# Kernel tuning notes

Measured on AMD Instinct MI355X. Metric: run time of the kernel, lower is better.

The kernel has to match this reference:

```python
import jax, jax.numpy as jnp
import numpy as np

HEADS, LEVELS, POINTS, DIMS = 8, 4, 4, 256
CH = DIMS // HEADS
SHAPES = np.array([[96, 96], [48, 48], [24, 24], [12, 12]], dtype=np.int64)
LEVEL_START = np.concatenate([[0], np.cumsum(SHAPES[:, 0] * SHAPES[:, 1])[:-1]]).astype(np.int64)
HW = int((SHAPES[:, 0] * SHAPES[:, 1]).sum())
N, Q = 2, HW


def setup_inputs() -> dict:
    key = jax.random.key(0)
    ks = jax.random.split(key, 8)
    return {
        "q": jax.random.normal(ks[0], (N, Q, DIMS), jnp.float32),
        "p": jax.random.uniform(ks[1], (N, Q, LEVELS, 2), jnp.float32),
        "v": jax.random.normal(ks[2], (N, HW, DIMS), jnp.float32),
        "W_off": jax.random.normal(ks[3], (DIMS, HEADS * LEVELS * POINTS * 2), jnp.float32) * 0.01,
        "b_off": jax.random.normal(ks[4], (HEADS * LEVELS * POINTS * 2,), jnp.float32) * 0.5,
        "W_attn": jax.random.normal(ks[5], (DIMS, HEADS * LEVELS * POINTS), jnp.float32) * 0.02,
        "b_attn": jnp.zeros((HEADS * LEVELS * POINTS,), jnp.float32),
        "W_in": jax.random.normal(ks[6], (DIMS, DIMS), jnp.float32) / np.float32(np.sqrt(DIMS)),
        "b_in": jnp.zeros((DIMS,), jnp.float32),
        "W_out": jax.random.normal(ks[7], (DIMS, DIMS), jnp.float32) / np.float32(np.sqrt(DIMS)),
        "b_out": jnp.zeros((DIMS,), jnp.float32),
        "shapes": jnp.asarray(SHAPES),
        "level_index": jnp.asarray(LEVEL_START),
    }


def _sample_level(vl, loc_l, Hl, Wl):
    """Bilinear sample with zero padding outside the feature map.
    vl: [N, Hl*Wl, heads, C]; loc_l: [N, Q, heads, P, 2] normalized (x, y) in [0,1].
    Returns [N, Q, P, heads, C]."""
    Nb, Qn, Hd, P, _ = loc_l.shape
    x = loc_l[..., 0] * Wl - 0.5  # pixel coords, align_corners=False convention
    y = loc_l[..., 1] * Hl - 0.5
    x0 = jnp.floor(x)
    y0 = jnp.floor(y)
    dx = x - x0
    dy = y - y0
    x0i = x0.astype(jnp.int32)
    y0i = y0.astype(jnp.int32)
    out = jnp.zeros((Nb, Qn, P, Hd, vl.shape[-1]), vl.dtype)
    corners = ((x0i, y0i, (1 - dx) * (1 - dy)), (x0i + 1, y0i, dx * (1 - dy)),
               (x0i, y0i + 1, (1 - dx) * dy), (x0i + 1, y0i + 1, dx * dy))
    for cx, cy, w in corners:
        valid = (cx >= 0) & (cx < Wl) & (cy >= 0) & (cy < Hl)
        idx = jnp.clip(cy, 0, Hl - 1) * Wl + jnp.clip(cx, 0, Wl - 1)  # [N,Q,Hd,P]
        idx_t = idx.transpose(0, 1, 3, 2).reshape(Nb, Qn * P, Hd, 1)
        g = jnp.take_along_axis(vl, idx_t, axis=1).reshape(Nb, Qn, P, Hd, -1)
        wv = jnp.where(valid, w, 0.0).transpose(0, 1, 3, 2)  # [N,Q,P,Hd]
        out = out + g * wv[..., None].astype(vl.dtype)
    return out


def _forward(q, p, v, W_off, b_off, W_attn, b_attn, W_in, b_in, W_out, b_out, shp, lsi):
    Nb, Qn, _ = q.shape
    v = (v @ W_in + b_in).reshape(Nb, -1, HEADS, CH)
    off = (q @ W_off + b_off).reshape(Nb, Qn, HEADS, LEVELS, POINTS, 2)
    attn = jax.nn.softmax((q @ W_attn + b_attn).reshape(Nb, Qn, HEADS, LEVELS * POINTS), axis=-1)
    attn = attn.reshape(Nb, Qn, HEADS, LEVELS, POINTS)
    # offsets normalized by (W, H) of each level, added to reference points (2-coord branch)
    off_norm = jnp.asarray(np.stack([shp[:, 1], shp[:, 0]], -1), q.dtype)  # [L, 2]
    loc = p[:, :, None, :, None, :] + off / off_norm[None, None, None, :, None, :]  # [N,Q,Hd,L,P,2]
    out = jnp.zeros((Nb, Qn, HEADS, CH), q.dtype)
    for l in range(LEVELS):
        Hl, Wl = int(shp[l, 0]), int(shp[l, 1])
        s = int(lsi[l])
        vl = jax.lax.slice_in_dim(v, s, s + Hl * Wl, axis=1)
        samp = _sample_level(vl, loc[:, :, :, l], Hl, Wl)  # [N,Q,P,Hd,C]
        out = out + jnp.einsum('nqphc,nqhp->nqhc', samp, attn[:, :, :, l])
    return out.reshape(Nb, Qn, DIMS) @ W_out + b_out


def reference(q, p, v, W_off, b_off, W_attn, b_attn, W_in, b_in, W_out, b_out, shapes, level_index):
    shp = np.asarray(shapes)  # spatial shapes are structural constants
    lsi = np.asarray(level_index)
    return _forward(q, p, v, W_off, b_off, W_attn, b_attn, W_in, b_in, W_out, b_out, shp, lsi)
```

## Files before the change

### kernel.cpp

```cpp
#include <hip/hip_runtime.h>
#include <hip/hip_bf16.h>
#include <math.h>

#define NB      2
#define QN      12240
#define HW_TOT  12240
#define DIMS    256
#define HEADS   8
#define CH      32
#define LEVELS  4
#define POINTS  4
#define M_TOT   (NB * QN)

typedef unsigned short ushort_t;
typedef __attribute__((ext_vector_type(8))) short short8;
typedef __attribute__((ext_vector_type(4))) float floatx4;

__device__ __forceinline__ ushort_t f2bf(float f) {
    __hip_bfloat16 h = __float2bfloat16(f);
    return *reinterpret_cast<ushort_t*>(&h);
}

__global__ __launch_bounds__(256) void convert_qv_kernel(
    const float* __restrict__ v, const float* __restrict__ q,
    ushort_t* __restrict__ vbf, ushort_t* __restrict__ qbf)
{
    const size_t i = ((size_t)blockIdx.x * 256 + threadIdx.x) * 8;
    const size_t half = (size_t)M_TOT * DIMS;
    const float* src; ushort_t* dst; size_t off;
    if (i < half) { src = v; dst = vbf; off = i; }
    else          { src = q; dst = qbf; off = i - half; }
    const float4 a = *(const float4*)&src[off];
    const float4 b = *(const float4*)&src[off + 4];
    ushort_t t[8] = {f2bf(a.x), f2bf(a.y), f2bf(a.z), f2bf(a.w),
                     f2bf(b.x), f2bf(b.y), f2bf(b.z), f2bf(b.w)};
    *(int4*)&dst[off] = *(int4*)t;
}

__global__ __launch_bounds__(256) void prep_weights_kernel(
    const float* __restrict__ W_in, const float* __restrict__ W_off,
    const float* __restrict__ W_attn, const float* __restrict__ W_out,
    const float* __restrict__ b_off, const float* __restrict__ b_attn,
    ushort_t* __restrict__ Tin, ushort_t* __restrict__ Tcomb,
    ushort_t* __restrict__ Tout, float* __restrict__ bcomb,
    int* __restrict__ vpad)
{
    const int z  = blockIdx.z;
    const int gi = blockIdx.x * 256 + threadIdx.x;
    if (z == 0 && gi < 32) vpad[gi] = 0;
    if (z == 1 && gi < 384)
        bcomb[gi] = (gi < 256) ? b_off[gi] : b_attn[gi - 256];
    const int Nw = (z == 1) ? 384 : 256;
    if (gi >= Nw * 256) return;
    const int k = gi & 255;
    const int n = gi >> 8;
    float val; ushort_t* T;
    if (z == 0)      { val = W_in[k * 256 + n];  T = Tin;  }
    else if (z == 1) { val = (n < 256) ? W_off[k * 256 + n]
                                       : W_attn[k * 128 + (n - 256)]; T = Tcomb; }
    else             { val = W_out[k * 256 + n]; T = Tout; }
    T[n * 256 + k] = f2bf(val);
}

__device__ __forceinline__ void gemm_tile_core(
    const ushort_t* __restrict__ A, const ushort_t* __restrict__ BT,
    const float* __restrict__ bias, void* __restrict__ C, bool c_bf16,
    int M, int Nc, int bm0, int bn0, int K,
    ushort_t* As, ushort_t* Bs)
{
    const int tid  = threadIdx.x;
    const int wave = tid >> 6;
    const int lane = tid & 63;
    const int quad = lane >> 4;
    const int l16  = lane & 15;
    const int wm   = (wave >> 1) * 64;
    const int wn   = (wave & 1) * 64;

    const int off0 = tid * 16;
    const int row0 = off0 >> 6;
    const int kc0  = (off0 & 63) >> 1;

    int ar0 = bm0 + row0;      if (ar0 > M - 1) ar0 = M - 1;
    int ar1 = bm0 + row0 + 64; if (ar1 > M - 1) ar1 = M - 1;

    const ushort_t* ga0 = A  + (size_t)ar0 * K + kc0;
    const ushort_t* ga1 = A  + (size_t)ar1 * K + kc0;
    const ushort_t* gb0 = BT + (size_t)(bn0 + row0) * K + kc0;
    const ushort_t* gb1 = BT + (size_t)(bn0 + row0 + 64) * K + kc0;

    ushort_t* lA0 = As + wave * 512;
    ushort_t* lA1 = As + wave * 512 + 2048;
    ushort_t* lB0 = Bs + wave * 512;
    ushort_t* lB1 = Bs + wave * 512 + 2048;

    floatx4 acc[4][4];
    #pragma unroll
    for (int i = 0; i < 4; ++i)
        #pragma unroll
        for (int j = 0; j < 4; ++j)
            acc[i][j] = (floatx4){0.f, 0.f, 0.f, 0.f};

    for (int kk = 0; kk < K; kk += 32) {
        __builtin_amdgcn_global_load_lds(
            (const __attribute__((address_space(1))) void*)(ga0 + kk),
            (__attribute__((address_space(3))) void*)lA0, 16, 0, 0);
        __builtin_amdgcn_global_load_lds(
            (const __attribute__((address_space(1))) void*)(ga1 + kk),
            (__attribute__((address_space(3))) void*)lA1, 16, 0, 0);
        __builtin_amdgcn_global_load_lds(
            (const __attribute__((address_space(1))) void*)(gb0 + kk),
            (__attribute__((address_space(3))) void*)lB0, 16, 0, 0);
        __builtin_amdgcn_global_load_lds(
            (const __attribute__((address_space(1))) void*)(gb1 + kk),
            (__attribute__((address_space(3))) void*)lB1, 16, 0, 0);
        __syncthreads();

        short8 af[4], bfr[4];
        #pragma unroll
        for (int mt = 0; mt < 4; ++mt)
            af[mt] = *(const short8*)&As[(wm + mt * 16 + l16) * 32 + quad * 8];
        #pragma unroll
        for (int nt = 0; nt < 4; ++nt)
            bfr[nt] = *(const short8*)&Bs[(wn + nt * 16 + l16) * 32 + quad * 8];
        #pragma unroll
        for (int mt = 0; mt < 4; ++mt)
            #pragma unroll
            for (int nt = 0; nt < 4; ++nt)
                acc[mt][nt] = __builtin_amdgcn_mfma_f32_16x16x32_bf16(
                    af[mt], bfr[nt], acc[mt][nt], 0, 0, 0);
        __syncthreads();
    }

    #pragma unroll
    for (int mt = 0; mt < 4; ++mt) {
        #pragma unroll
        for (int j = 0; j < 4; ++j) {
            const int row = bm0 + wm + mt * 16 + quad * 4 + j;
            if (row >= M) continue;
            #pragma unroll
            for (int nt = 0; nt < 4; ++nt) {
                const int col = bn0 + wn + nt * 16 + l16;
                const float val = acc[mt][nt][j] + bias[col];
                if (c_bf16) {
                    const size_t idx = (((size_t)(col >> 5) * M + row) << 5) + (col & 31);
                    ((ushort_t*)C)[idx] = f2bf(val);
                } else {
                    ((float*)C)[(size_t)row * Nc + col] = val;
                }
            }
        }
    }
}

__global__ __launch_bounds__(256) void gemm_proj_kernel(
    const ushort_t* __restrict__ vbf, const ushort_t* __restrict__ qbf,
    const ushort_t* __restrict__ Tin, const ushort_t* __restrict__ Tcomb,
    const float* __restrict__ b_in, const float* __restrict__ bcomb,
    ushort_t* __restrict__ vproj, float* __restrict__ offlog)
{
    __shared__ ushort_t As[128 * 32];
    __shared__ ushort_t Bs[128 * 32];
    const int bm0 = blockIdx.x * 128;
    const int y = blockIdx.y;
    if (y < 2)
        gemm_tile_core(vbf, Tin, b_in, vproj, true, M_TOT, 256, bm0, y * 128, 256, As, Bs);
    else
        gemm_tile_core(qbf, Tcomb, bcomb, offlog, false, M_TOT, 384, bm0, (y - 2) * 128, 256, As, Bs);
}

__global__ __launch_bounds__(256) void gemm_out_kernel(
    const ushort_t* __restrict__ mid, const ushort_t* __restrict__ Tout,
    const float* __restrict__ b_out, float* __restrict__ out)
{
    __shared__ ushort_t As[128 * 32];
    __shared__ ushort_t Bs[128 * 32];
    gemm_tile_core(mid, Tout, b_out, out, false, M_TOT, 256,
                   blockIdx.x * 128, blockIdx.y * 128, 256, As, Bs);
}

#define LO32(u) __uint_as_float((u) << 16)
#define HI32(u) __uint_as_float((u) & 0xffff0000u)
#define ACC8(W, g) \
    a0 = fmaf(W, LO32(g.x), a0);  a1 = fmaf(W, HI32(g.x), a1); \
    a2 = fmaf(W, LO32(g.y), a2);  a3 = fmaf(W, HI32(g.y), a3); \
    a4 = fmaf(W, LO32(g.z), a4);  a5 = fmaf(W, HI32(g.z), a5); \
    a6 = fmaf(W, LO32(g.w), a6);  a7 = fmaf(W, HI32(g.w), a7);

__global__ __launch_bounds__(256, 8) void msda_sample_kernel(
    const ushort_t* __restrict__ vproj, const float* __restrict__ offlog,
    const float* __restrict__ p, ushort_t* __restrict__ mid)
{
    __shared__ int s_buf[4096];

    const int tid = threadIdx.x;
    const int wv  = tid >> 6;
    const int l   = tid & 63;
    const int nq  = blockIdx.x * 4 + wv;
    const int nb  = (nq >= QN) ? 1 : 0;
    const int wbase = wv * 1024;

    const size_t orow = (size_t)nq * 384;
    const float2 off0 = *(const float2*)&offlog[orow + 2 * l];
    const float2 off1 = *(const float2*)&offlog[orow + 128 + 2 * l];
    const float  lg0  = offlog[orow + 256 + l];
    const float  lg1  = offlog[orow + 320 + l];
    const int    lvl  = (l >> 2) & 3;
    const float2 pl   = *(const float2*)&p[(size_t)nq * 8 + lvl * 2];

    float m0 = lg0, m1 = lg1;
    #pragma unroll
    for (int m = 8; m; m >>= 1) {
        m0 = fmaxf(m0, __shfl_xor(m0, m));
        m1 = fmaxf(m1, __shfl_xor(m1, m));
    }
    const float e0 = __expf(lg0 - m0);
    const float e1 = __expf(lg1 - m1);
    float s0 = e0, s1 = e1;
    #pragma unroll
    for (int m = 8; m; m >>= 1) {
        s0 += __shfl_xor(s0, m);
        s1 += __shfl_xor(s1, m);
    }
    const float wt0 = e0 * __builtin_amdgcn_rcpf(s0);
    const float wt1 = e1 * __builtin_amdgcn_rcpf(s1);

    const int   Wl  = 96 >> lvl;
    const float fW  = (float)Wl;
    const int   st  = 12288 - (12288 >> (2 * lvl));
    const int   h4  = l >> 4;

    #pragma unroll
    for (int set = 0; set < 2; ++set) {
        const float ox = set ? off1.x : off0.x;
        const float oy = set ? off1.y : off0.y;
        const float wt = set ? wt1 : wt0;
        const int   h  = set ? (h4 + 4) : h4;

        const float x  = fmaf(pl.x, fW, ox) - 0.5f;
        const float y  = fmaf(pl.y, fW, oy) - 0.5f;
        const float xf = floorf(x), yf = floorf(y);
        const float dx = x - xf,    dy = y - yf;
        const int   x0 = (int)xf,   y0 = (int)yf;
        const bool vxl = (unsigned)x0       < (unsigned)Wl;
        const bool vxr = (unsigned)(x0 + 1) < (unsigned)Wl;
        const bool vy0 = (unsigned)y0       < (unsigned)Wl;
        const bool vy1 = (unsigned)(y0 + 1) < (unsigned)Wl;

        const float wxl = vxl ? (1.0f - dx) : (vxr ? dx : 0.0f);
        const float wxr = (vxl && vxr) ? dx : 0.0f;
        const int   xb  = vxl ? x0 : 0;

        const float wy0f = wt * (1.0f - dy), wy1f = wt * dy;
        const float w_l0 = vy0 ? wxl * wy0f : 0.0f;
        const float w_r0 = vy0 ? wxr * wy0f : 0.0f;
        const float w_l1 = vy1 ? wxl * wy1f : 0.0f;
        const float w_r1 = vy1 ? wxr * wy1f : 0.0f;

        int yc0 = y0;     if (yc0 < 0) yc0 = 0; if (yc0 > Wl - 1) yc0 = Wl - 1;
        int yc1 = y0 + 1; if (yc1 < 0) yc1 = 0; if (yc1 > Wl - 1) yc1 = Wl - 1;

        const int rowb = h * M_TOT + nb * HW_TOT + st + xb;
        const int lin0 = rowb + yc0 * Wl;
        const int lin1 = rowb + yc1 * Wl;

        const int a  = l * 16 + set * 8;
        const int ph = (a ^ (((a >> 8) & 3) << 2)) + wbase;
        *(int4*)&s_buf[ph] = (int4){lin0 << 6, __float_as_int(w_l0),
                                    __float_as_int(w_r0), lin1 << 6};
        *(int2*)&s_buf[ph ^ 4] = (int2){__float_as_int(w_l1), __float_as_int(w_r1)};
    }

    __builtin_amdgcn_wave_barrier();
    asm volatile("s_waitcnt lgkmcnt(0)" ::: "memory");
    __builtin_amdgcn_wave_barrier();

    const int  h    = l >> 3;
    const int  c16  = (l & 7) * 16;
    const bool hicn = (l & 4) != 0;
    const int  rbas = (h & 3) * 256 + (h >> 2) * 8;
    const char* __restrict__ vb = (const char*)vproj;

    float a0 = 0.f, a1 = 0.f, a2 = 0.f, a3 = 0.f;
    float a4 = 0.f, a5 = 0.f, a6 = 0.f, a7 = 0.f;

    #pragma unroll 2
    for (int t = 0; t < 16; ++t) {
        const int ia = rbas + t * 16;
        const int ph = (ia ^ (((ia >> 8) & 3) << 2)) + wbase;
        const int4 cA = *(const int4*)&s_buf[ph];
        const int2 cB = *(const int2*)&s_buf[ph ^ 4];
        const uint4 g0 = *(const uint4*)(vb + (unsigned)(cA.x + c16));
        const uint4 g1 = *(const uint4*)(vb + (unsigned)(cA.w + c16));
        const float w0 = hicn ? __int_as_float(cA.z) : __int_as_float(cA.y);
        const float w1 = hicn ? __int_as_float(cB.y) : __int_as_float(cB.x);
        ACC8(w0, g0);
        ACC8(w1, g1);
    }

    a0 += __shfl_xor(a0, 4);  a1 += __shfl_xor(a1, 4);
    a2 += __shfl_xor(a2, 4);  a3 += __shfl_xor(a3, 4);
    a4 += __shfl_xor(a4, 4);  a5 += __shfl_xor(a5, 4);
    a6 += __shfl_xor(a6, 4);  a7 += __shfl_xor(a7, 4);

    const float o0 = hicn ? a4 : a0;
    const float o1 = hicn ? a5 : a1;
    const float o2 = hicn ? a6 : a2;
    const float o3 = hicn ? a7 : a3;
    ushort_t mv[4] = {f2bf(o0), f2bf(o1), f2bf(o2), f2bf(o3)};
    const int col = h * 32 + (l & 3) * 8 + (l & 4);
    *(uint2*)&mid[(size_t)nq * 256 + col] = *(uint2*)mv;
}

extern "C" void kernel_launch(void* const* d_in, const int* in_sizes, int n_in,
                              void* d_out, int out_size, void* d_ws, size_t ws_size,
                              hipStream_t stream)
{
    const float* q      = (const float*)d_in[0];
    const float* p      = (const float*)d_in[1];
    const float* v      = (const float*)d_in[2];
    const float* W_off  = (const float*)d_in[3];
    const float* b_off  = (const float*)d_in[4];
    const float* W_attn = (const float*)d_in[5];
    const float* b_attn = (const float*)d_in[6];
    const float* W_in   = (const float*)d_in[7];
    const float* b_in   = (const float*)d_in[8];
    const float* W_out  = (const float*)d_in[9];
    const float* b_out  = (const float*)d_in[10];
    float* out = (float*)d_out;

    const int M = M_TOT;

    ushort_t* vproj  = (ushort_t*)d_ws;
    ushort_t* vpad   = vproj + (size_t)M * 256;
    float*    offlog = (float*)(vpad + 64);
    ushort_t* vbf    = (ushort_t*)(offlog + (size_t)M * 384);
    ushort_t* mid    = vbf;
    ushort_t* qbf    = vbf + (size_t)M * 256;
    ushort_t* Tin    = qbf + (size_t)M * 256;
    ushort_t* Tcomb  = Tin + 256 * 256;
    ushort_t* Tout   = Tcomb + 384 * 256;
    float*    bcomb  = (float*)(Tout + 256 * 256);

    convert_qv_kernel<<<dim3(6120), 256, 0, stream>>>(v, q, vbf, qbf);
    prep_weights_kernel<<<dim3(384, 1, 3), 256, 0, stream>>>(
        W_in, W_off, W_attn, W_out, b_off, b_attn, Tin, Tcomb, Tout, bcomb,
        (int*)vpad);

    gemm_proj_kernel<<<dim3(192, 5), 256, 0, stream>>>(
        vbf, qbf, Tin, Tcomb, b_in, bcomb, vproj, offlog);
    msda_sample_kernel<<<dim3(M / 4), 256, 0, stream>>>(vproj, offlog, p, mid);
    gemm_out_kernel<<<dim3(192, 2), 256, 0, stream>>>(mid, Tout, b_out, out);
}
```

Measured before the change: 188.7 us.

## Fuse prep kernels, store offsets in fp16, split sampling by head halves

Merges the activation conversion and weight-prep launches into one kernel. The offset/logit projection is now written as fp16 instead of fp32, halving that intermediate's traffic. The sampling kernel is restructured so each block handles half the heads for four queries, doubling the grid, with a padded shared layout and one gather per lane per iteration instead of two. Storing offsets in fp16 loses precision in the sampling coordinates, and the extra shuffle reduction adds work.

```diff
diff --git a/kernel.cpp b/kernel.cpp
--- a/kernel.cpp
+++ b/kernel.cpp
@@ -1,5 +1,6 @@
 #include <hip/hip_runtime.h>
 #include <hip/hip_bf16.h>
+#include <hip/hip_fp16.h>
 #include <math.h>
 
 #define NB      2
@@ -20,24 +21,14 @@
     __hip_bfloat16 h = __float2bfloat16(f);
     return *reinterpret_cast<ushort_t*>(&h);
 }
-
-__global__ __launch_bounds__(256) void convert_qv_kernel(
+__device__ __forceinline__ ushort_t f2h(float f) {
+    __half h = __float2half(f);
+    return *reinterpret_cast<ushort_t*>(&h);
+}
+
+__global__ __launch_bounds__(256) void convert_prep_kernel(
     const float* __restrict__ v, const float* __restrict__ q,
-    ushort_t* __restrict__ vbf, ushort_t* __restrict__ qbf)
-{
-    const size_t i = ((size_t)blockIdx.x * 256 + threadIdx.x) * 8;
-    const size_t half = (size_t)M_TOT * DIMS;
-    const float* src; ushort_t* dst; size_t off;
-    if (i < half) { src = v; dst = vbf; off = i; }
-    else          { src = q; dst = qbf; off = i - half; }
-    const float4 a = *(const float4*)&src[off];
-    const float4 b = *(const float4*)&src[off + 4];
-    ushort_t t[8] = {f2bf(a.x), f2bf(a.y), f2bf(a.z), f2bf(a.w),
-                     f2bf(b.x), f2bf(b.y), f2bf(b.z), f2bf(b.w)};
-    *(int4*)&dst[off] = *(int4*)t;
-}
-
-__global__ __launch_bounds__(256) void prep_weights_kernel(
+    ushort_t* __restrict__ vbf, ushort_t* __restrict__ qbf,
     const float* __restrict__ W_in, const float* __restrict__ W_off,
     const float* __restrict__ W_attn, const float* __restrict__ W_out,
     const float* __restrict__ b_off, const float* __restrict__ b_attn,
@@ -45,26 +36,41 @@
     ushort_t* __restrict__ Tout, float* __restrict__ bcomb,
     int* __restrict__ vpad)
 {
-    const int z  = blockIdx.z;
-    const int gi = blockIdx.x * 256 + threadIdx.x;
-    if (z == 0 && gi < 32) vpad[gi] = 0;
-    if (z == 1 && gi < 384)
-        bcomb[gi] = (gi < 256) ? b_off[gi] : b_attn[gi - 256];
-    const int Nw = (z == 1) ? 384 : 256;
-    if (gi >= Nw * 256) return;
+    const int bx  = blockIdx.x;
+    const int tid = threadIdx.x;
+    if (bx < 6120) {
+        const size_t i = ((size_t)bx * 256 + tid) * 8;
+        const size_t half = (size_t)M_TOT * DIMS;
+        const float* src; ushort_t* dst; size_t off;
+        if (i < half) { src = v; dst = vbf; off = i; }
+        else          { src = q; dst = qbf; off = i - half; }
+        const float4 a = *(const float4*)&src[off];
+        const float4 b = *(const float4*)&src[off + 4];
+        ushort_t t[8] = {f2bf(a.x), f2bf(a.y), f2bf(a.z), f2bf(a.w),
+                         f2bf(b.x), f2bf(b.y), f2bf(b.z), f2bf(b.w)};
+        *(int4*)&dst[off] = *(int4*)t;
+        return;
+    }
+    const int bi = bx - 6120;
+    const int gi = bi * 256 + tid;
+    if (gi < 32)  vpad[gi] = 0;
+    if (gi < 384) bcomb[gi] = (gi < 256) ? b_off[gi] : b_attn[gi - 256];
     const int k = gi & 255;
     const int n = gi >> 8;
-    float val; ushort_t* T;
-    if (z == 0)      { val = W_in[k * 256 + n];  T = Tin;  }
-    else if (z == 1) { val = (n < 256) ? W_off[k * 256 + n]
-                                       : W_attn[k * 128 + (n - 256)]; T = Tcomb; }
-    else             { val = W_out[k * 256 + n]; T = Tout; }
-    T[n * 256 + k] = f2bf(val);
+    if (gi < 65536) {
+        Tin[n * 256 + k]  = f2bf(W_in[k * 256 + n]);
+        Tout[n * 256 + k] = f2bf(W_out[k * 256 + n]);
+    }
+    {
+        const float val = (n < 256) ? W_off[k * 256 + n]
+                                    : W_attn[k * 128 + (n - 256)];
+        Tcomb[n * 256 + k] = f2bf(val);
+    }
 }
 
 __device__ __forceinline__ void gemm_tile_core(
     const ushort_t* __restrict__ A, const ushort_t* __restrict__ BT,
-    const float* __restrict__ bias, void* __restrict__ C, bool c_bf16,
+    const float* __restrict__ bias, void* __restrict__ C, int cmode,
     int M, int Nc, int bm0, int bn0, int K,
     ushort_t* As, ushort_t* Bs)
 {
@@ -141,9 +147,11 @@
             for (int nt = 0; nt < 4; ++nt) {
                 const int col = bn0 + wn + nt * 16 + l16;
                 const float val = acc[mt][nt][j] + bias[col];
-                if (c_bf16) {
+                if (cmode == 1) {
                     const size_t idx = (((size_t)(col >> 5) * M + row) << 5) + (col & 31);
                     ((ushort_t*)C)[idx] = f2bf(val);
+                } else if (cmode == 2) {
+                    ((ushort_t*)C)[(size_t)row * Nc + col] = f2h(val);
                 } else {
                     ((float*)C)[(size_t)row * Nc + col] = val;
                 }
@@ -156,16 +164,16 @@
     const ushort_t* __restrict__ vbf, const ushort_t* __restrict__ qbf,
     const ushort_t* __restrict__ Tin, const ushort_t* __restrict__ Tcomb,
     const float* __restrict__ b_in, const float* __restrict__ bcomb,
-    ushort_t* __restrict__ vproj, float* __restrict__ offlog)
+    ushort_t* __restrict__ vproj, ushort_t* __restrict__ offh)
 {
     __shared__ ushort_t As[128 * 32];
     __shared__ ushort_t Bs[128 * 32];
     const int bm0 = blockIdx.x * 128;
     const int y = blockIdx.y;
     if (y < 2)
-        gemm_tile_core(vbf, Tin, b_in, vproj, true, M_TOT, 256, bm0, y * 128, 256, As, Bs);
+        gemm_tile_core(vbf, Tin, b_in, vproj, 1, M_TOT, 256, bm0, y * 128, 256, As, Bs);
     else
-        gemm_tile_core(qbf, Tcomb, bcomb, offlog, false, M_TOT, 384, bm0, (y - 2) * 128, 256, As, Bs);
+        gemm_tile_core(qbf, Tcomb, bcomb, offh, 2, M_TOT, 384, bm0, (y - 2) * 128, 256, As, Bs);
 }
 
 __global__ __launch_bounds__(256) void gemm_out_kernel(
@@ -174,7 +182,7 @@
 {
     __shared__ ushort_t As[128 * 32];
     __shared__ ushort_t Bs[128 * 32];
-    gemm_tile_core(mid, Tout, b_out, out, false, M_TOT, 256,
+    gemm_tile_core(mid, Tout, b_out, out, 0, M_TOT, 256,
                    blockIdx.x * 128, blockIdx.y * 128, 256, As, Bs);
 }
 
@@ -187,57 +195,48 @@
     a6 = fmaf(W, LO32(g.w), a6);  a7 = fmaf(W, HI32(g.w), a7);
 
 __global__ __launch_bounds__(256, 8) void msda_sample_kernel(
-    const ushort_t* __restrict__ vproj, const float* __restrict__ offlog,
+    const ushort_t* __restrict__ vproj, const ushort_t* __restrict__ offh,
     const float* __restrict__ p, ushort_t* __restrict__ mid)
 {
-    __shared__ int s_buf[4096];
+    __shared__ int4 s_main[4][68];
+    __shared__ int2 s_aux[4][68];
 
     const int tid = threadIdx.x;
     const int wv  = tid >> 6;
     const int l   = tid & 63;
-    const int nq  = blockIdx.x * 4 + wv;
+    const int idx = blockIdx.x;
+    const int b8  = idx & 7;
+    const int hh  = b8 >> 2;
+    const int qg  = (idx >> 3) * 4 + (b8 & 3);
+    const int nq  = qg * 4 + wv;
     const int nb  = (nq >= QN) ? 1 : 0;
-    const int wbase = wv * 1024;
 
     const size_t orow = (size_t)nq * 384;
-    const float2 off0 = *(const float2*)&offlog[orow + 2 * l];
-    const float2 off1 = *(const float2*)&offlog[orow + 128 + 2 * l];
-    const float  lg0  = offlog[orow + 256 + l];
-    const float  lg1  = offlog[orow + 320 + l];
-    const int    lvl  = (l >> 2) & 3;
-    const float2 pl   = *(const float2*)&p[(size_t)nq * 8 + lvl * 2];
-
-    float m0 = lg0, m1 = lg1;
+    const __half2 o2 = *(const __half2*)&offh[orow + hh * 128 + 2 * l];
+    const float2  of = __half22float2(o2);
+    const float   lg = __half2float(
+        *(const __half*)&offh[orow + 256 + hh * 64 + l]);
+    const int     lvl = (l >> 2) & 3;
+    const float2  pl  = *(const float2*)&p[(size_t)nq * 8 + lvl * 2];
+
+    float mx = lg;
     #pragma unroll
-    for (int m = 8; m; m >>= 1) {
-        m0 = fmaxf(m0, __shfl_xor(m0, m));
-        m1 = fmaxf(m1, __shfl_xor(m1, m));
-    }
-    const float e0 = __expf(lg0 - m0);
-    const float e1 = __expf(lg1 - m1);
-    float s0 = e0, s1 = e1;
+    for (int m = 8; m; m >>= 1) mx = fmaxf(mx, __shfl_xor(mx, m));
+    const float e = __expf(lg - mx);
+    float ss = e;
     #pragma unroll
-    for (int m = 8; m; m >>= 1) {
-        s0 += __shfl_xor(s0, m);
-        s1 += __shfl_xor(s1, m);
-    }
-    const float wt0 = e0 * __builtin_amdgcn_rcpf(s0);
-    const float wt1 = e1 * __builtin_amdgcn_rcpf(s1);
-
-    const int   Wl  = 96 >> lvl;
-    const float fW  = (float)Wl;
-    const int   st  = 12288 - (12288 >> (2 * lvl));
-    const int   h4  = l >> 4;
-
-    #pragma unroll
-    for (int set = 0; set < 2; ++set) {
-        const float ox = set ? off1.x : off0.x;
-        const float oy = set ? off1.y : off0.y;
-        const float wt = set ? wt1 : wt0;
-        const int   h  = set ? (h4 + 4) : h4;
-
-        const float x  = fmaf(pl.x, fW, ox) - 0.5f;
-        const float y  = fmaf(pl.y, fW, oy) - 0.5f;
+    for (int m = 8; m; m >>= 1) ss += __shfl_xor(ss, m);
+    const float wt = e * __builtin_amdgcn_rcpf(ss);
+
+    const int   Wl = 96 >> lvl;
+    const float fW = (float)Wl;
+    const int   st = 12288 - (12288 >> (2 * lvl));
+    const int   h4 = l >> 4;
+    const int   h  = hh * 4 + h4;
+
+    {
+        const float x  = fmaf(pl.x, fW, of.x) - 0.5f;
+        const float y  = fmaf(pl.y, fW, of.y) - 0.5f;
         const float xf = floorf(x), yf = floorf(y);
         const float dx = x - xf,    dy = y - yf;
         const int   x0 = (int)xf,   y0 = (int)yf;
@@ -262,53 +261,53 @@
         const int rowb = h * M_TOT + nb * HW_TOT + st + xb;
         const int lin0 = rowb + yc0 * Wl;
         const int lin1 = rowb + yc1 * Wl;
-
-        const int a  = l * 16 + set * 8;
-        const int ph = (a ^ (((a >> 8) & 3) << 2)) + wbase;
-        *(int4*)&s_buf[ph] = (int4){lin0 << 6, __float_as_int(w_l0),
-                                    __float_as_int(w_r0), lin1 << 6};
-        *(int2*)&s_buf[ph ^ 4] = (int2){__float_as_int(w_l1), __float_as_int(w_r1)};
+        const int e17 = h4 * 17 + (l & 15);
+        s_main[wv][e17] = (int4){lin0 << 6, __float_as_int(w_l0),
+                                 __float_as_int(w_r0), lin1 << 6};
+        s_aux[wv][e17]  = (int2){__float_as_int(w_l1), __float_as_int(w_r1)};
     }
 
     __builtin_amdgcn_wave_barrier();
     asm volatile("s_waitcnt lgkmcnt(0)" ::: "memory");
     __builtin_amdgcn_wave_barrier();
 
-    const int  h    = l >> 3;
-    const int  c16  = (l & 7) * 16;
-    const bool hicn = (l & 4) != 0;
-    const int  rbas = (h & 3) * 256 + (h >> 2) * 8;
+    const int hg     = l >> 4;
+    const int rowr   = (l >> 3) & 1;
+    const int corner = (l >> 2) & 1;
+    const int c16    = (l & 7) * 16;
     const char* __restrict__ vb = (const char*)vproj;
 
     float a0 = 0.f, a1 = 0.f, a2 = 0.f, a3 = 0.f;
     float a4 = 0.f, a5 = 0.f, a6 = 0.f, a7 = 0.f;
 
-    #pragma unroll 2
+    #pragma unroll 4
     for (int t = 0; t < 16; ++t) {
-        const int ia = rbas + t * 16;
-        const int ph = (ia ^ (((ia >> 8) & 3) << 2)) + wbase;
-        const int4 cA = *(const int4*)&s_buf[ph];
-        const int2 cB = *(const int2*)&s_buf[ph ^ 4];
-        const uint4 g0 = *(const uint4*)(vb + (unsigned)(cA.x + c16));
-        const uint4 g1 = *(const uint4*)(vb + (unsigned)(cA.w + c16));
-        const float w0 = hicn ? __int_as_float(cA.z) : __int_as_float(cA.y);
-        const float w1 = hicn ? __int_as_float(cB.y) : __int_as_float(cB.x);
-        ACC8(w0, g0);
-        ACC8(w1, g1);
+        const int  e17 = hg * 17 + t;
+        const int4 c   = s_main[wv][e17];
+        const int2 cb  = s_aux[wv][e17];
+        const int  base = rowr ? c.w : c.x;
+        const float wl  = rowr ? __int_as_float(cb.x) : __int_as_float(c.y);
+        const float wr  = rowr ? __int_as_float(cb.y) : __int_as_float(c.z);
+        const float w   = corner ? wr : wl;
+        const uint4 g   = *(const uint4*)(vb + (unsigned)(base + c16));
+        ACC8(w, g);
     }
 
     a0 += __shfl_xor(a0, 4);  a1 += __shfl_xor(a1, 4);
     a2 += __shfl_xor(a2, 4);  a3 += __shfl_xor(a3, 4);
     a4 += __shfl_xor(a4, 4);  a5 += __shfl_xor(a5, 4);
     a6 += __shfl_xor(a6, 4);  a7 += __shfl_xor(a7, 4);
-
-    const float o0 = hicn ? a4 : a0;
-    const float o1 = hicn ? a5 : a1;
-    const float o2 = hicn ? a6 : a2;
-    const float o3 = hicn ? a7 : a3;
-    ushort_t mv[4] = {f2bf(o0), f2bf(o1), f2bf(o2), f2bf(o3)};
-    const int col = h * 32 + (l & 3) * 8 + (l & 4);
-    *(uint2*)&mid[(size_t)nq * 256 + col] = *(uint2*)mv;
+    a0 += __shfl_xor(a0, 8);  a1 += __shfl_xor(a1, 8);
+    a2 += __shfl_xor(a2, 8);  a3 += __shfl_xor(a3, 8);
+    a4 += __shfl_xor(a4, 8);  a5 += __shfl_xor(a5, 8);
+    a6 += __shfl_xor(a6, 8);  a7 += __shfl_xor(a7, 8);
+
+    if ((l & 12) == 0) {
+        ushort_t mv[8] = {f2bf(a0), f2bf(a1), f2bf(a2), f2bf(a3),
+                          f2bf(a4), f2bf(a5), f2bf(a6), f2bf(a7)};
+        const int col = (hh * 4 + hg) * 32 + (l & 3) * 8;
+        *(uint4*)&mid[(size_t)nq * 256 + col] = *(uint4*)mv;
+    }
 }
 
 extern "C" void kernel_launch(void* const* d_in, const int* in_sizes, int n_in,
@@ -332,8 +331,8 @@
 
     ushort_t* vproj  = (ushort_t*)d_ws;
     ushort_t* vpad   = vproj + (size_t)M * 256;
-    float*    offlog = (float*)(vpad + 64);
-    ushort_t* vbf    = (ushort_t*)(offlog + (size_t)M * 384);
+    ushort_t* offh   = vpad + 64;
+    ushort_t* vbf    = offh + (size_t)M * 384;
     ushort_t* mid    = vbf;
     ushort_t* qbf    = vbf + (size_t)M * 256;
     ushort_t* Tin    = qbf + (size_t)M * 256;
@@ -341,13 +340,12 @@
     ushort_t* Tout   = Tcomb + 384 * 256;
     float*    bcomb  = (float*)(Tout + 256 * 256);
 
-    convert_qv_kernel<<<dim3(6120), 256, 0, stream>>>(v, q, vbf, qbf);
-    prep_weights_kernel<<<dim3(384, 1, 3), 256, 0, stream>>>(
-        W_in, W_off, W_attn, W_out, b_off, b_attn, Tin, Tcomb, Tout, bcomb,
-        (int*)vpad);
+    convert_prep_kernel<<<dim3(6504), 256, 0, stream>>>(
+        v, q, vbf, qbf, W_in, W_off, W_attn, W_out, b_off, b_attn,
+        Tin, Tcomb, Tout, bcomb, (int*)vpad);
 
     gemm_proj_kernel<<<dim3(192, 5), 256, 0, stream>>>(
-        vbf, qbf, Tin, Tcomb, b_in, bcomb, vproj, offlog);
-    msda_sample_kernel<<<dim3(M / 4), 256, 0, stream>>>(vproj, offlog, p, mid);
+        vbf, qbf, Tin, Tcomb, b_in, bcomb, vproj, offh);
+    msda_sample_kernel<<<dim3(12240), 256, 0, stream>>>(vproj, offh, p, mid);
     gemm_out_kernel<<<dim3(192, 2), 256, 0, stream>>>(mid, Tout, b_out, out);
 }
```

New measurement: 179.9 us. 1.05x faster.
